# Kernel tuning notes

Hardware: AMD Instinct MI355X
Metric: run time of the kernel (lower is better)

## Reference

```python
import jax, jax.numpy as jnp
import numpy as np

N = 100000      # nodes
E = 1600000     # edges (avg degree 16)
IN = 128        # in_channels
H = 128         # hidden
C = 40          # num_classes
NCOMM = 1000    # number of communities


def setup_inputs() -> dict:
    key = jax.random.key(0)
    ks = jax.random.split(key, 6)
    x = jax.random.normal(ks[0], (N, IN), dtype=jnp.float32)
    edge_index = jax.random.randint(ks[1], (2, E), 0, N, dtype=jnp.int64)
    community = jax.random.randint(ks[2], (N,), 0, NCOMM, dtype=jnp.int64)
    W_in = jax.random.normal(ks[3], (2 * IN, H), dtype=jnp.float32) * 0.05
    b_in = jnp.zeros((H,), dtype=jnp.float32)
    W1 = jax.random.normal(ks[4], (H, H), dtype=jnp.float32) * 0.05
    b1 = jnp.zeros((H,), dtype=jnp.float32)
    W2 = jax.random.normal(ks[5], (H, C), dtype=jnp.float32) * 0.05
    b2 = jnp.zeros((C,), dtype=jnp.float32)
    return {"x": x, "edge_index": edge_index, "community": community,
            "W_in": W_in, "b_in": b_in, "W1": W1, "b1": b1, "W2": W2, "b2": b2}


def _gcn_conv(h, W, b, src, dst, n):
    """PyG GCNConv: transform, add self-loops, symmetric deg^-1/2 normalization."""
    hw = h @ W  # [n, out]
    deg = jax.ops.segment_sum(jnp.ones((src.shape[0],), hw.dtype), dst, num_segments=n) + 1.0  # +1 self-loop
    dis = jax.lax.rsqrt(deg)                      # deg >= 1 always
    norm = dis[src] * dis[dst]                    # [E]
    agg = jax.ops.segment_sum(hw[src] * norm[:, None], dst, num_segments=n)
    # self-loop contribution: norm_ii = dis[i]^2 = 1/deg[i]
    return agg + hw * (1.0 / deg)[:, None] + b


def reference(x, edge_index, community, W_in, b_in, W1, b1, W2, b2):
    n = x.shape[0]
    # CommunityPassing(aggr='mean'): per-community mean, broadcast back to nodes
    csum = jax.ops.segment_sum(x, community, num_segments=NCOMM)
    ccnt = jax.ops.segment_sum(jnp.ones((n,), x.dtype), community, num_segments=NCOMM)
    cmean = csum / jnp.maximum(ccnt, 1.0)[:, None]
    x_comm = cmean[community]                     # [n, IN]
    h = jnp.concatenate([x, x_comm], axis=-1)     # [n, 2*IN]
    h = jax.nn.relu(h @ W_in + b_in)              # dropout is identity at eval
    src, dst = edge_index[0], edge_index[1]
    h = jax.nn.relu(_gcn_conv(h, W1, b1, src, dst, n))
    out = _gcn_conv(h, W2, b2, src, dst, n)
    return out
```

## Files before the change

### kernel.cpp

```cpp
#include <hip/hip_runtime.h>
#include <cstdint>
#include <cstddef>

#define NNODES 100000
#define NEDGES 1600000
#define INCH   128
#define HID    128
#define NCLS   40
#define NCOMM_ 1000

typedef unsigned int uint32;
typedef unsigned short ushort16;
typedef short s16x8 __attribute__((ext_vector_type(8)));
typedef float f32x4 __attribute__((ext_vector_type(4)));

static __device__ __forceinline__ float4 ld4(const float* p){ return *reinterpret_cast<const float4*>(p); }

static __device__ __forceinline__ unsigned short f2b(float f){
  union{float f; uint32 u;} v; v.f=f;
  uint32 r = v.u + 0x7fffu + ((v.u>>16)&1u);
  return (unsigned short)(r>>16);
}
static __device__ __forceinline__ float b2f(unsigned short h){
  union{uint32 u; float f;} v; v.u = ((uint32)h)<<16; return v.f;
}
static __device__ __forceinline__ float lo16f(uint32 u){ return __int_as_float((int)(u<<16)); }
static __device__ __forceinline__ float hi16f(uint32 u){ return __int_as_float((int)(u&0xffff0000u)); }

static __device__ __forceinline__ void acc8(float* a, uint4 v, float nr){
  a[0]=fmaf(lo16f(v.x),nr,a[0]); a[1]=fmaf(hi16f(v.x),nr,a[1]);
  a[2]=fmaf(lo16f(v.y),nr,a[2]); a[3]=fmaf(hi16f(v.y),nr,a[3]);
  a[4]=fmaf(lo16f(v.z),nr,a[4]); a[5]=fmaf(hi16f(v.z),nr,a[5]);
  a[6]=fmaf(lo16f(v.w),nr,a[6]); a[7]=fmaf(hi16f(v.w),nr,a[7]);
}
static __device__ __forceinline__ void acc4(float* a, uint2 v, float nr){
  a[0]=fmaf(lo16f(v.x),nr,a[0]); a[1]=fmaf(hi16f(v.x),nr,a[1]);
  a[2]=fmaf(lo16f(v.y),nr,a[2]); a[3]=fmaf(hi16f(v.y),nr,a[3]);
}

__global__ void k_count(const int* __restrict__ ei, int* __restrict__ deg,
                        const int* __restrict__ comm, int* __restrict__ ccnt){
  int idx = blockIdx.x*blockDim.x + threadIdx.x;
  if (idx < NEDGES) atomicAdd(&deg[ei[NEDGES + idx]], 1);
  if (idx < NNODES) atomicAdd(&ccnt[comm[idx]], 1);
}

__global__ void k_scan1(const int* __restrict__ in, int n, int* __restrict__ part){
  int t=threadIdx.x, b=blockIdx.x;
  int base=b*1024+t*4, s=0;
  #pragma unroll
  for(int j=0;j<4;j++){ int i=base+j; if(i<n) s+=in[i]; }
  #pragma unroll
  for(int off=32;off>0;off>>=1) s+=__shfl_down(s,off,64);
  __shared__ int wm[4];
  if((t&63)==0) wm[t>>6]=s;
  __syncthreads();
  if(t==0) part[b]=wm[0]+wm[1]+wm[2]+wm[3];
}

__global__ void k_scan2(int* __restrict__ part, int P){
  __shared__ int sm[256];
  int t=threadIdx.x;
  int v=(t<P)?part[t]:0;
  sm[t]=v; __syncthreads();
  #pragma unroll
  for(int off=1;off<256;off<<=1){
    int u=(t>=off)?sm[t-off]:0;
    __syncthreads();
    sm[t]+=u;
    __syncthreads();
  }
  if(t<P) part[t]=(t==0)?0:sm[t-1];
  if(t==0) part[P]=sm[255];
}

__global__ void k_scan3(const int* __restrict__ in, int n, const int* __restrict__ part, int P,
                        int* __restrict__ out){
  int t=threadIdx.x,b=blockIdx.x;
  int base=b*1024+t*4;
  int v[4], ts=0;
  #pragma unroll
  for(int j=0;j<4;j++){ v[j]=(base+j<n)?in[base+j]:0; ts+=v[j]; }
  int lane=t&63, w=t>>6, sc=ts;
  #pragma unroll
  for(int off=1;off<64;off<<=1){ int u=__shfl_up(sc,off,64); if(lane>=off) sc+=u; }
  __shared__ int wm[4];
  if(lane==63) wm[w]=sc;
  __syncthreads();
  int woff=0;
  for(int i=0;i<w;i++) woff+=wm[i];
  int pos=part[b]+woff+sc-ts;
  #pragma unroll
  for(int j=0;j<4;j++){ if(base+j<n) out[base+j]=pos; pos+=v[j]; }
  if(b==0 && t==0) out[n]=part[P];
}

__global__ void k_nodeprep(const int* __restrict__ deg, float* __restrict__ dis, float* __restrict__ dinv){
  int i=blockIdx.x*blockDim.x+threadIdx.x;
  if(i<NNODES){ float d=(float)(deg[i]+1); dis[i]=rsqrtf(d); dinv[i]=1.0f/d; }
}

__global__ void k_fill_edges(const int* __restrict__ ei, const int* __restrict__ rp, int* __restrict__ fill,
                             const float* __restrict__ dis, int2* __restrict__ ep){
  int e=blockIdx.x*blockDim.x+threadIdx.x;
  if(e<NEDGES){
    int s=ei[e], d=ei[NEDGES+e];
    int p=rp[d]+atomicAdd(&fill[d],1);
    ep[p]=make_int2(s, __float_as_int(dis[s]));
  }
}

__global__ void k_fill_comm(const int* __restrict__ comm, const int* __restrict__ crow, int* __restrict__ cfill,
                            int* __restrict__ cnode){
  int i=blockIdx.x*blockDim.x+threadIdx.x;
  if(i<NNODES){
    int c=comm[i];
    int p=crow[c]+atomicAdd(&cfill[c],1);
    cnode[p]=i;
  }
}

__global__ void k_comm_mean(const float* __restrict__ x, const int* __restrict__ crow,
                            const int* __restrict__ cnode, float* __restrict__ cmean){
  int c=blockIdx.x; int f=threadIdx.x;
  int a=crow[c], b=crow[c+1];
  float s=0.f;
  for(int j=a;j<b;j++){
    int nd=cnode[j];
    s += x[(size_t)nd*INCH + f];
  }
  float cnt=(float)(b-a);
  cmean[(size_t)c*INCH + f] = s / fmaxf(cnt,1.0f);
}

__global__ void k_wprep(const float* __restrict__ W_in, const float* __restrict__ W1, const float* __restrict__ W2,
                        ushort16* __restrict__ Wt0h, ushort16* __restrict__ Wt0l,
                        ushort16* __restrict__ Wt1h, ushort16* __restrict__ Wt1l,
                        ushort16* __restrict__ Wt2h, ushort16* __restrict__ Wt2l){
  int t = blockIdx.x*256 + threadIdx.x;
  float v; ushort16* ph; ushort16* pl; int off;
  if(t < 32768){
    int n=t>>8, k=t&255; v=W_in[k*128+n]; ph=Wt0h; pl=Wt0l; off=t;
  } else if(t < 49152){
    int u=t-32768; int n=u>>7, k=u&127; v=W1[k*128+n]; ph=Wt1h; pl=Wt1l; off=u;
  } else if(t < 55296){
    int u=t-49152; int n=u>>7, k=u&127; v=(n<40)?W2[k*40+n]:0.f; ph=Wt2h; pl=Wt2l; off=u;
  } else return;
  unsigned short h=f2b(v); unsigned short lo=f2b(v-b2f(h));
  ph[off]=h; pl[off]=lo;
}

template<int K, bool CONCAT, bool BIAS, bool RELU>
__global__ __launch_bounds__(256) void k_mm128(const void* __restrict__ A0, const float* __restrict__ A1f,
                                               const int* __restrict__ comm,
                                               const ushort16* __restrict__ WtH, const ushort16* __restrict__ WtL,
                                               const float* __restrict__ bias,
                                               ushort16* __restrict__ out, int M){
  __shared__ __align__(16) ushort16 As[128*40];
  __shared__ __align__(16) ushort16 Bh[128*40];
  __shared__ __align__(16) ushort16 Bl[128*40];
  int t=threadIdx.x;
  int m0=blockIdx.x*128;
  int lane=t&63, w=t>>6;
  int g=lane>>4, r15=lane&15;

  f32x4 acc0[8], acc1[8];
  #pragma unroll
  for(int i=0;i<8;i++){ acc0[i]=(f32x4){0,0,0,0}; acc1[i]=(f32x4){0,0,0,0}; }

  int ar = t>>1, ko = (t&1)*16;

  for(int kc=0;kc<K;kc+=32){
    __syncthreads();
    {
      s16x8 q0, q1;
      int gr = m0 + ar;
      if(gr < M){
        if(CONCAT){
          const float* src = (kc<128) ? ((const float*)A0 + (size_t)gr*128 + kc + ko)
                                      : (A1f + (size_t)comm[gr]*128 + (kc-128) + ko);
          float4 p0=ld4(src), p1=ld4(src+4), p2=ld4(src+8), p3=ld4(src+12);
          q0[0]=(short)f2b(p0.x); q0[1]=(short)f2b(p0.y); q0[2]=(short)f2b(p0.z); q0[3]=(short)f2b(p0.w);
          q0[4]=(short)f2b(p1.x); q0[5]=(short)f2b(p1.y); q0[6]=(short)f2b(p1.z); q0[7]=(short)f2b(p1.w);
          q1[0]=(short)f2b(p2.x); q1[1]=(short)f2b(p2.y); q1[2]=(short)f2b(p2.z); q1[3]=(short)f2b(p2.w);
          q1[4]=(short)f2b(p3.x); q1[5]=(short)f2b(p3.y); q1[6]=(short)f2b(p3.z); q1[7]=(short)f2b(p3.w);
        } else {
          const ushort16* srcu = (const ushort16*)A0 + (size_t)gr*K + kc + ko;
          q0 = *(const s16x8*)srcu;
          q1 = *(const s16x8*)(srcu+8);
        }
      } else {
        q0=(s16x8){0,0,0,0,0,0,0,0}; q1=q0;
      }
      ushort16* dst=&As[ar*40+ko];
      *(s16x8*)dst=q0; *(s16x8*)(dst+8)=q1;
    }
    {
      const ushort16* sh=&WtH[(size_t)ar*K + kc + ko];
      s16x8 b0=*(const s16x8*)sh, b1=*(const s16x8*)(sh+8);
      ushort16* dh=&Bh[ar*40+ko];
      *(s16x8*)dh=b0; *(s16x8*)(dh+8)=b1;
      const ushort16* sl=&WtL[(size_t)ar*K + kc + ko];
      s16x8 c0=*(const s16x8*)sl, c1=*(const s16x8*)(sl+8);
      ushort16* dl=&Bl[ar*40+ko];
      *(s16x8*)dl=c0; *(s16x8*)(dl+8)=c1;
    }
    __syncthreads();
    s16x8 a0 = *(const s16x8*)&As[(w*32      + r15)*40 + g*8];
    s16x8 a1 = *(const s16x8*)&As[(w*32 + 16 + r15)*40 + g*8];
    #pragma unroll
    for(int tn=0;tn<8;tn++){
      s16x8 bh = *(const s16x8*)&Bh[(tn*16 + r15)*40 + g*8];
      s16x8 bl = *(const s16x8*)&Bl[(tn*16 + r15)*40 + g*8];
      acc0[tn] = __builtin_amdgcn_mfma_f32_16x16x32_bf16(a0, bh, acc0[tn], 0,0,0);
      acc0[tn] = __builtin_amdgcn_mfma_f32_16x16x32_bf16(a0, bl, acc0[tn], 0,0,0);
      acc1[tn] = __builtin_amdgcn_mfma_f32_16x16x32_bf16(a1, bh, acc1[tn], 0,0,0);
      acc1[tn] = __builtin_amdgcn_mfma_f32_16x16x32_bf16(a1, bl, acc1[tn], 0,0,0);
    }
  }

  #pragma unroll
  for(int tn=0;tn<8;tn++){
    int col = tn*16 + r15;
    float bv = BIAS ? bias[col] : 0.f;
    #pragma unroll
    for(int rr=0;rr<4;rr++){
      int row0 = m0 + w*32 + g*4 + rr;
      if(row0 < M){
        float v = acc0[tn][rr] + bv;
        if(RELU) v = fmaxf(v, 0.f);
        out[(size_t)row0*128 + col] = f2b(v);
      }
      int row1 = m0 + w*32 + 16 + g*4 + rr;
      if(row1 < M){
        float v = acc1[tn][rr] + bv;
        if(RELU) v = fmaxf(v, 0.f);
        out[(size_t)row1*128 + col] = f2b(v);
      }
    }
  }
}

__global__ __launch_bounds__(256) void k_mm40(const ushort16* __restrict__ A0,
                                              const ushort16* __restrict__ WtH, const ushort16* __restrict__ WtL,
                                              ushort16* __restrict__ out, int M){
  __shared__ __align__(16) ushort16 As[128*40];
  __shared__ __align__(16) ushort16 Bh[48*40];
  __shared__ __align__(16) ushort16 Bl[48*40];
  int t=threadIdx.x;
  int m0=blockIdx.x*128;
  int lane=t&63, w=t>>6;
  int g=lane>>4, r15=lane&15;

  f32x4 acc0[3], acc1[3];
  #pragma unroll
  for(int i=0;i<3;i++){ acc0[i]=(f32x4){0,0,0,0}; acc1[i]=(f32x4){0,0,0,0}; }

  int ar=t>>1, ko=(t&1)*16;

  for(int kc=0;kc<128;kc+=32){
    __syncthreads();
    {
      s16x8 q0,q1;
      int gr=m0+ar;
      if(gr<M){
        const ushort16* srcu = A0 + (size_t)gr*128 + kc + ko;
        q0=*(const s16x8*)srcu; q1=*(const s16x8*)(srcu+8);
      } else { q0=(s16x8){0,0,0,0,0,0,0,0}; q1=q0; }
      ushort16* dst=&As[ar*40+ko];
      *(s16x8*)dst=q0; *(s16x8*)(dst+8)=q1;
    }
    if(t<96){
      int n=t>>1, k2=(t&1)*16;
      const ushort16* sh=&WtH[(size_t)n*128 + kc + k2];
      s16x8 b0=*(const s16x8*)sh, b1=*(const s16x8*)(sh+8);
      ushort16* dh=&Bh[n*40+k2];
      *(s16x8*)dh=b0; *(s16x8*)(dh+8)=b1;
    } else if(t<192){
      int u=t-96; int n=u>>1, k2=(u&1)*16;
      const ushort16* sl=&WtL[(size_t)n*128 + kc + k2];
      s16x8 c0=*(const s16x8*)sl, c1=*(const s16x8*)(sl+8);
      ushort16* dl=&Bl[n*40+k2];
      *(s16x8*)dl=c0; *(s16x8*)(dl+8)=c1;
    }
    __syncthreads();
    s16x8 a0=*(const s16x8*)&As[(w*32      + r15)*40 + g*8];
    s16x8 a1=*(const s16x8*)&As[(w*32 + 16 + r15)*40 + g*8];
    #pragma unroll
    for(int tn=0;tn<3;tn++){
      s16x8 bh=*(const s16x8*)&Bh[(tn*16 + r15)*40 + g*8];
      s16x8 bl=*(const s16x8*)&Bl[(tn*16 + r15)*40 + g*8];
      acc0[tn]=__builtin_amdgcn_mfma_f32_16x16x32_bf16(a0,bh,acc0[tn],0,0,0);
      acc0[tn]=__builtin_amdgcn_mfma_f32_16x16x32_bf16(a0,bl,acc0[tn],0,0,0);
      acc1[tn]=__builtin_amdgcn_mfma_f32_16x16x32_bf16(a1,bh,acc1[tn],0,0,0);
      acc1[tn]=__builtin_amdgcn_mfma_f32_16x16x32_bf16(a1,bl,acc1[tn],0,0,0);
    }
  }
  #pragma unroll
  for(int tn=0;tn<3;tn++){
    int col=tn*16+r15;
    if(col<NCLS){
      #pragma unroll
      for(int rr=0;rr<4;rr++){
        int row0=m0+w*32+g*4+rr;
        if(row0<M) out[(size_t)row0*NCLS+col]=f2b(acc0[tn][rr]);
        int row1=m0+w*32+16+g*4+rr;
        if(row1<M) out[(size_t)row1*NCLS+col]=f2b(acc1[tn][rr]);
      }
    }
  }
}

__global__ __launch_bounds__(256) void k_agg_h(const uint4* __restrict__ hwv, const int* __restrict__ rp,
                                               const int2* __restrict__ ep,
                                               const float* __restrict__ dis, const float* __restrict__ dinv,
                                               const float* __restrict__ bias, uint4* __restrict__ h1v){
  int w=threadIdx.x>>6;
  int i=blockIdx.x*4+w;
  if(i>=NNODES) return;
  int lane=threadIdx.x&63;
  int g=lane>>4, f=lane&15;
  int e0=rp[i], e1=rp[i+1];
  float di=dis[i];
  float a[8]={0,0,0,0,0,0,0,0};
  int e=e0+g;
  for(; e+4<e1; e+=8){
    int2 r0=ep[e], r1=ep[e+4];
    float n0=di*__int_as_float(r0.y), n1=di*__int_as_float(r1.y);
    uint4 v0=hwv[(size_t)r0.x*16+f];
    uint4 v1=hwv[(size_t)r1.x*16+f];
    acc8(a,v0,n0); acc8(a,v1,n1);
  }
  if(e<e1){
    int2 r0=ep[e];
    float n0=di*__int_as_float(r0.y);
    uint4 v0=hwv[(size_t)r0.x*16+f];
    acc8(a,v0,n0);
  }
  #pragma unroll
  for(int k=0;k<8;k++){
    a[k]+=__shfl_xor(a[k],16);
    a[k]+=__shfl_xor(a[k],32);
  }
  if(g==0){
    uint4 sv=hwv[(size_t)i*16+f];
    float dv=dinv[i];
    float4 bA=*reinterpret_cast<const float4*>(&bias[8*f]);
    float4 bB=*reinterpret_cast<const float4*>(&bias[8*f+4]);
    float o0=fmaxf(fmaf(lo16f(sv.x),dv,a[0])+bA.x,0.f);
    float o1=fmaxf(fmaf(hi16f(sv.x),dv,a[1])+bA.y,0.f);
    float o2=fmaxf(fmaf(lo16f(sv.y),dv,a[2])+bA.z,0.f);
    float o3=fmaxf(fmaf(hi16f(sv.y),dv,a[3])+bA.w,0.f);
    float o4=fmaxf(fmaf(lo16f(sv.z),dv,a[4])+bB.x,0.f);
    float o5=fmaxf(fmaf(hi16f(sv.z),dv,a[5])+bB.y,0.f);
    float o6=fmaxf(fmaf(lo16f(sv.w),dv,a[6])+bB.z,0.f);
    float o7=fmaxf(fmaf(hi16f(sv.w),dv,a[7])+bB.w,0.f);
    uint4 o;
    o.x=((uint32)f2b(o1)<<16)|(uint32)f2b(o0);
    o.y=((uint32)f2b(o3)<<16)|(uint32)f2b(o2);
    o.z=((uint32)f2b(o5)<<16)|(uint32)f2b(o4);
    o.w=((uint32)f2b(o7)<<16)|(uint32)f2b(o6);
    h1v[(size_t)i*16+f]=o;
  }
}

__global__ __launch_bounds__(256) void k_agg_out(const uint2* __restrict__ hv, const int* __restrict__ rp,
                                                 const int2* __restrict__ ep,
                                                 const float* __restrict__ dis, const float* __restrict__ dinv,
                                                 const float* __restrict__ bias, float* __restrict__ out){
  int w=threadIdx.x>>6;
  int i=blockIdx.x*4+w;
  if(i>=NNODES) return;
  int lane=threadIdx.x&63;
  int g=lane>>4, f=lane&15;
  bool act=(f<10);
  int e0=rp[i], e1=rp[i+1];
  float di=dis[i];
  float a[4]={0,0,0,0};
  int e=e0+g;
  for(; e+4<e1; e+=8){
    int2 r0=ep[e], r1=ep[e+4];
    float n0=di*__int_as_float(r0.y), n1=di*__int_as_float(r1.y);
    if(act){
      uint2 v0=hv[(size_t)r0.x*10+f];
      uint2 v1=hv[(size_t)r1.x*10+f];
      acc4(a,v0,n0); acc4(a,v1,n1);
    }
  }
  if(e<e1){
    int2 r0=ep[e];
    float n0=di*__int_as_float(r0.y);
    if(act){
      uint2 v0=hv[(size_t)r0.x*10+f];
      acc4(a,v0,n0);
    }
  }
  #pragma unroll
  for(int k=0;k<4;k++){
    a[k]+=__shfl_xor(a[k],16);
    a[k]+=__shfl_xor(a[k],32);
  }
  if(g==0 && act){
    uint2 sv=hv[(size_t)i*10+f];
    float dv=dinv[i];
    float4 b=*reinterpret_cast<const float4*>(&bias[4*f]);
    float4 o;
    o.x=fmaf(lo16f(sv.x),dv,a[0])+b.x;
    o.y=fmaf(hi16f(sv.x),dv,a[1])+b.y;
    o.z=fmaf(lo16f(sv.y),dv,a[2])+b.z;
    o.w=fmaf(hi16f(sv.y),dv,a[3])+b.w;
    *reinterpret_cast<float4*>(&out[(size_t)i*40+4*f])=o;
  }
}

extern "C" void kernel_launch(void* const* d_in, const int* in_sizes, int n_in,
                              void* d_out, int out_size, void* d_ws, size_t ws_size,
                              hipStream_t stream) {
  const float* x    = (const float*)d_in[0];
  const int*   ei   = (const int*)  d_in[1];
  const int*   comm = (const int*)  d_in[2];
  const float* W_in = (const float*)d_in[3];
  const float* b_in = (const float*)d_in[4];
  const float* W1   = (const float*)d_in[5];
  const float* b1   = (const float*)d_in[6];
  const float* W2   = (const float*)d_in[7];
  const float* b2   = (const float*)d_in[8];
  float* out = (float*)d_out;

  char* base=(char*)d_ws; size_t off=0;
  auto alloc=[&](size_t bytes)->void*{ void* p=base+off; off=(off+bytes+255)&~(size_t)255; return p; };

  int* zz    =(int*)alloc((size_t)(2*NNODES+2*NCOMM_)*4);
  int* deg_i = zz;
  int* fill  = zz + NNODES;
  int* ccnt  = zz + 2*NNODES;
  int* cfill = zz + 2*NNODES + NCOMM_;
  int* rp    =(int*)alloc((size_t)(NNODES+1)*4);
  int* crow  =(int*)alloc((size_t)(NCOMM_+1)*4);
  int* partA =(int*)alloc(260*4);
  int* partB =(int*)alloc(16*4);
  int2* ep   =(int2*)alloc((size_t)NEDGES*8);
  int* cnode =(int*)alloc((size_t)NNODES*4);
  float* dis =(float*)alloc((size_t)NNODES*4);
  float* dinv=(float*)alloc((size_t)NNODES*4);
  float* cmean=(float*)alloc((size_t)NCOMM_*INCH*4);
  ushort16* h0 =(ushort16*)alloc((size_t)NNODES*HID*2);
  ushort16* hw =(ushort16*)alloc((size_t)NNODES*HID*2);
  ushort16* Wt0h=(ushort16*)alloc(32768*2);
  ushort16* Wt0l=(ushort16*)alloc(32768*2);
  ushort16* Wt1h=(ushort16*)alloc(16384*2);
  ushort16* Wt1l=(ushort16*)alloc(16384*2);
  ushort16* Wt2h=(ushort16*)alloc(6144*2);
  ushort16* Wt2l=(ushort16*)alloc(6144*2);

  hipMemsetAsync(zz, 0, (size_t)(2*NNODES+2*NCOMM_)*4, stream);

  int gE=(NEDGES+255)/256, gN=(NNODES+255)/256;
  k_count<<<gE,256,0,stream>>>(ei, deg_i, comm, ccnt);

  int PA=(NNODES+1023)/1024;
  k_scan1<<<PA,256,0,stream>>>(deg_i, NNODES, partA);
  k_scan2<<<1,256,0,stream>>>(partA, PA);
  k_scan3<<<PA,256,0,stream>>>(deg_i, NNODES, partA, PA, rp);

  int PB=(NCOMM_+1023)/1024;
  k_scan1<<<PB,256,0,stream>>>(ccnt, NCOMM_, partB);
  k_scan2<<<1,256,0,stream>>>(partB, PB);
  k_scan3<<<PB,256,0,stream>>>(ccnt, NCOMM_, partB, PB, crow);

  k_nodeprep<<<gN,256,0,stream>>>(deg_i, dis, dinv);
  k_fill_edges<<<gE,256,0,stream>>>(ei, rp, fill, dis, ep);
  k_fill_comm<<<gN,256,0,stream>>>(comm, crow, cfill, cnode);
  k_comm_mean<<<NCOMM_,128,0,stream>>>(x, crow, cnode, cmean);
  k_wprep<<<216,256,0,stream>>>(W_in, W1, W2, Wt0h, Wt0l, Wt1h, Wt1l, Wt2h, Wt2l);

  int gM=(NNODES+127)/128;
  k_mm128<256,true,true,true><<<gM,256,0,stream>>>(x, cmean, comm, Wt0h, Wt0l, b_in, h0, NNODES);
  k_mm128<128,false,false,false><<<gM,256,0,stream>>>(h0, nullptr, nullptr, Wt1h, Wt1l, nullptr, hw, NNODES);
  int gA=(NNODES+3)/4;
  k_agg_h<<<gA,256,0,stream>>>((const uint4*)hw, rp, ep, dis, dinv, b1, (uint4*)h0);
  k_mm40<<<gM,256,0,stream>>>(h0, Wt2h, Wt2l, hw, NNODES);
  k_agg_out<<<gA,256,0,stream>>>((const uint2*)hw, rp, ep, dis, dinv, b2, out);
}
```

Before: 535.0 us.

## Build CSR via two-level bucketed counting sort instead of global atomics

Replaces the global-atomic degree count, node-level scan and atomic edge scatter with a bucket counting sort. Edges are first histogrammed per block into 256-node buckets in shared memory, scanned, and scattered into bucket order. A per-bucket kernel then builds the local CSR, degrees and normalisation with shared-memory atomics. Edge records shrink from (src, dis) pairs to src only, with dis[src] gathered in the aggregation kernels, which trades smaller edge reads for an extra dependent load. The build adds a serial single-block scan and an intermediate edge buffer pass.

```diff
diff --git a/kernel.cpp b/kernel.cpp
--- a/kernel.cpp
+++ b/kernel.cpp
@@ -9,6 +9,11 @@
 #define NCLS   40
 #define NCOMM_ 1000
 
+#define NBLK  128
+#define EPB   (NEDGES/NBLK)
+#define NBUCK ((NNODES+255)/256)
+#define NCNT  (NBLK*NBUCK)
+
 typedef unsigned int uint32;
 typedef unsigned short ushort16;
 typedef short s16x8 __attribute__((ext_vector_type(8)));
@@ -38,11 +43,109 @@
   a[2]=fmaf(lo16f(v.y),nr,a[2]); a[3]=fmaf(hi16f(v.y),nr,a[3]);
 }
 
-__global__ void k_count(const int* __restrict__ ei, int* __restrict__ deg,
-                        const int* __restrict__ comm, int* __restrict__ ccnt){
-  int idx = blockIdx.x*blockDim.x + threadIdx.x;
-  if (idx < NEDGES) atomicAdd(&deg[ei[NEDGES + idx]], 1);
-  if (idx < NNODES) atomicAdd(&ccnt[comm[idx]], 1);
+__global__ void k_ccomm(const int* __restrict__ comm, int* __restrict__ ccnt){
+  int i=blockIdx.x*blockDim.x+threadIdx.x;
+  if(i<NNODES) atomicAdd(&ccnt[comm[i]],1);
+}
+
+__global__ __launch_bounds__(256) void k_bcnt(const int* __restrict__ ei, int* __restrict__ cnt){
+  __shared__ int h[NBUCK];
+  int t=threadIdx.x, blk=blockIdx.x;
+  for(int i=t;i<NBUCK;i+=256) h[i]=0;
+  __syncthreads();
+  int base=blk*EPB;
+  for(int j=t;j<EPB;j+=256){
+    int d=ei[NEDGES+base+j];
+    atomicAdd(&h[d>>8],1);
+  }
+  __syncthreads();
+  for(int i=t;i<NBUCK;i+=256) cnt[i*NBLK+blk]=h[i];
+}
+
+__global__ __launch_bounds__(1024) void k_bscan(int* __restrict__ cnt, int* __restrict__ brow,
+                                                int* __restrict__ rp){
+  __shared__ int sm[1024];
+  int t=threadIdx.x;
+  const int span=(NCNT+1023)/1024;
+  int base=t*span;
+  int s=0;
+  for(int j=0;j<span;j++){ int i=base+j; if(i<NCNT) s+=cnt[i]; }
+  sm[t]=s; __syncthreads();
+  #pragma unroll
+  for(int off=1;off<1024;off<<=1){
+    int u=(t>=off)?sm[t-off]:0;
+    __syncthreads();
+    sm[t]+=u;
+    __syncthreads();
+  }
+  int run=(t==0)?0:sm[t-1];
+  for(int j=0;j<span;j++){
+    int i=base+j;
+    if(i<NCNT){
+      int c=cnt[i];
+      cnt[i]=run;
+      if((i&(NBLK-1))==0) brow[i/NBLK]=run;
+      run+=c;
+    }
+  }
+  if(t==1023){ brow[NBUCK]=NEDGES; rp[NNODES]=NEDGES; }
+}
+
+__global__ __launch_bounds__(256) void k_bscatter(const int* __restrict__ ei, const int* __restrict__ cnt,
+                                                  int2* __restrict__ ebuf){
+  __shared__ int offs[NBUCK];
+  int t=threadIdx.x, blk=blockIdx.x;
+  for(int i=t;i<NBUCK;i+=256) offs[i]=cnt[i*NBLK+blk];
+  __syncthreads();
+  int base=blk*EPB;
+  for(int j=t;j<EPB;j+=256){
+    int e=base+j;
+    int s=ei[e], d=ei[NEDGES+e];
+    int p=atomicAdd(&offs[d>>8],1);
+    ebuf[p]=make_int2(s,d);
+  }
+}
+
+__global__ __launch_bounds__(256) void k_bcsr(const int2* __restrict__ ebuf, const int* __restrict__ brow,
+                                              int* __restrict__ rp, float* __restrict__ dis,
+                                              float* __restrict__ dinv, int* __restrict__ esrc){
+  __shared__ int lcnt[256], lrp[256], lfill[256];
+  int b=blockIdx.x, t=threadIdx.x;
+  int e0=brow[b], e1=brow[b+1];
+  int n0=b*256, nloc=min(256, NNODES-n0);
+  lcnt[t]=0;
+  __syncthreads();
+  for(int e=e0+t;e<e1;e+=256){
+    int d=ebuf[e].y;
+    atomicAdd(&lcnt[d&255],1);
+  }
+  __syncthreads();
+  lrp[t]=lcnt[t]; __syncthreads();
+  #pragma unroll
+  for(int off=1;off<256;off<<=1){
+    int u=(t>=off)?lrp[t-off]:0;
+    __syncthreads();
+    lrp[t]+=u;
+    __syncthreads();
+  }
+  int excl=lrp[t]-lcnt[t];
+  __syncthreads();
+  lrp[t]=e0+excl;
+  lfill[t]=0;
+  if(t<nloc){
+    int gid=n0+t;
+    rp[gid]=e0+excl;
+    float dd=(float)(lcnt[t]+1);
+    dis[gid]=rsqrtf(dd);
+    dinv[gid]=1.0f/dd;
+  }
+  __syncthreads();
+  for(int e=e0+t;e<e1;e+=256){
+    int2 r=ebuf[e];
+    int lr=r.y&255;
+    int slot=atomicAdd(&lfill[lr],1);
+    esrc[lrp[lr]+slot]=r.x;
+  }
 }
 
 __global__ void k_scan1(const int* __restrict__ in, int n, int* __restrict__ part){
@@ -93,21 +196,6 @@
   #pragma unroll
   for(int j=0;j<4;j++){ if(base+j<n) out[base+j]=pos; pos+=v[j]; }
   if(b==0 && t==0) out[n]=part[P];
-}
-
-__global__ void k_nodeprep(const int* __restrict__ deg, float* __restrict__ dis, float* __restrict__ dinv){
-  int i=blockIdx.x*blockDim.x+threadIdx.x;
-  if(i<NNODES){ float d=(float)(deg[i]+1); dis[i]=rsqrtf(d); dinv[i]=1.0f/d; }
-}
-
-__global__ void k_fill_edges(const int* __restrict__ ei, const int* __restrict__ rp, int* __restrict__ fill,
-                             const float* __restrict__ dis, int2* __restrict__ ep){
-  int e=blockIdx.x*blockDim.x+threadIdx.x;
-  if(e<NEDGES){
-    int s=ei[e], d=ei[NEDGES+e];
-    int p=rp[d]+atomicAdd(&fill[d],1);
-    ep[p]=make_int2(s, __float_as_int(dis[s]));
-  }
 }
 
 __global__ void k_fill_comm(const int* __restrict__ comm, const int* __restrict__ crow, int* __restrict__ cfill,
@@ -312,7 +400,7 @@
 }
 
 __global__ __launch_bounds__(256) void k_agg_h(const uint4* __restrict__ hwv, const int* __restrict__ rp,
-                                               const int2* __restrict__ ep,
+                                               const int* __restrict__ esrc,
                                                const float* __restrict__ dis, const float* __restrict__ dinv,
                                                const float* __restrict__ bias, uint4* __restrict__ h1v){
   int w=threadIdx.x>>6;
@@ -325,16 +413,16 @@
   float a[8]={0,0,0,0,0,0,0,0};
   int e=e0+g;
   for(; e+4<e1; e+=8){
-    int2 r0=ep[e], r1=ep[e+4];
-    float n0=di*__int_as_float(r0.y), n1=di*__int_as_float(r1.y);
-    uint4 v0=hwv[(size_t)r0.x*16+f];
-    uint4 v1=hwv[(size_t)r1.x*16+f];
+    int s0=esrc[e], s1=esrc[e+4];
+    float n0=di*dis[s0], n1=di*dis[s1];
+    uint4 v0=hwv[(size_t)s0*16+f];
+    uint4 v1=hwv[(size_t)s1*16+f];
     acc8(a,v0,n0); acc8(a,v1,n1);
   }
   if(e<e1){
-    int2 r0=ep[e];
-    float n0=di*__int_as_float(r0.y);
-    uint4 v0=hwv[(size_t)r0.x*16+f];
+    int s0=esrc[e];
+    float n0=di*dis[s0];
+    uint4 v0=hwv[(size_t)s0*16+f];
     acc8(a,v0,n0);
   }
   #pragma unroll
@@ -365,7 +453,7 @@
 }
 
 __global__ __launch_bounds__(256) void k_agg_out(const uint2* __restrict__ hv, const int* __restrict__ rp,
-                                                 const int2* __restrict__ ep,
+                                                 const int* __restrict__ esrc,
                                                  const float* __restrict__ dis, const float* __restrict__ dinv,
                                                  const float* __restrict__ bias, float* __restrict__ out){
   int w=threadIdx.x>>6;
@@ -379,19 +467,19 @@
   float a[4]={0,0,0,0};
   int e=e0+g;
   for(; e+4<e1; e+=8){
-    int2 r0=ep[e], r1=ep[e+4];
-    float n0=di*__int_as_float(r0.y), n1=di*__int_as_float(r1.y);
+    int s0=esrc[e], s1=esrc[e+4];
+    float n0=di*dis[s0], n1=di*dis[s1];
     if(act){
-      uint2 v0=hv[(size_t)r0.x*10+f];
-      uint2 v1=hv[(size_t)r1.x*10+f];
+      uint2 v0=hv[(size_t)s0*10+f];
+      uint2 v1=hv[(size_t)s1*10+f];
       acc4(a,v0,n0); acc4(a,v1,n1);
     }
   }
   if(e<e1){
-    int2 r0=ep[e];
-    float n0=di*__int_as_float(r0.y);
+    int s0=esrc[e];
+    float n0=di*dis[s0];
     if(act){
-      uint2 v0=hv[(size_t)r0.x*10+f];
+      uint2 v0=hv[(size_t)s0*10+f];
       acc4(a,v0,n0);
     }
   }
@@ -430,16 +518,16 @@
   char* base=(char*)d_ws; size_t off=0;
   auto alloc=[&](size_t bytes)->void*{ void* p=base+off; off=(off+bytes+255)&~(size_t)255; return p; };
 
-  int* zz    =(int*)alloc((size_t)(2*NNODES+2*NCOMM_)*4);
-  int* deg_i = zz;
-  int* fill  = zz + NNODES;
-  int* ccnt  = zz + 2*NNODES;
-  int* cfill = zz + 2*NNODES + NCOMM_;
+  int* zz    =(int*)alloc((size_t)(2*NCOMM_)*4);
+  int* ccnt  = zz;
+  int* cfill = zz + NCOMM_;
+  int* cnt   =(int*)alloc((size_t)NCNT*4);
+  int* brow  =(int*)alloc((size_t)(NBUCK+1)*4);
   int* rp    =(int*)alloc((size_t)(NNODES+1)*4);
   int* crow  =(int*)alloc((size_t)(NCOMM_+1)*4);
-  int* partA =(int*)alloc(260*4);
   int* partB =(int*)alloc(16*4);
-  int2* ep   =(int2*)alloc((size_t)NEDGES*8);
+  int2* ebuf =(int2*)alloc((size_t)NEDGES*8);
+  int* esrc  =(int*)alloc((size_t)NEDGES*4);
   int* cnode =(int*)alloc((size_t)NNODES*4);
   float* dis =(float*)alloc((size_t)NNODES*4);
   float* dinv=(float*)alloc((size_t)NNODES*4);
@@ -453,23 +541,20 @@
   ushort16* Wt2h=(ushort16*)alloc(6144*2);
   ushort16* Wt2l=(ushort16*)alloc(6144*2);
 
-  hipMemsetAsync(zz, 0, (size_t)(2*NNODES+2*NCOMM_)*4, stream);
-
-  int gE=(NEDGES+255)/256, gN=(NNODES+255)/256;
-  k_count<<<gE,256,0,stream>>>(ei, deg_i, comm, ccnt);
-
-  int PA=(NNODES+1023)/1024;
-  k_scan1<<<PA,256,0,stream>>>(deg_i, NNODES, partA);
-  k_scan2<<<1,256,0,stream>>>(partA, PA);
-  k_scan3<<<PA,256,0,stream>>>(deg_i, NNODES, partA, PA, rp);
-
+  hipMemsetAsync(zz, 0, (size_t)(2*NCOMM_)*4, stream);
+
+  int gN=(NNODES+255)/256;
+
+  k_bcnt    <<<NBLK,256,0,stream>>>(ei, cnt);
+  k_bscan   <<<1,1024,0,stream>>>(cnt, brow, rp);
+  k_bscatter<<<NBLK,256,0,stream>>>(ei, cnt, ebuf);
+  k_bcsr    <<<NBUCK,256,0,stream>>>(ebuf, brow, rp, dis, dinv, esrc);
+
+  k_ccomm<<<gN,256,0,stream>>>(comm, ccnt);
   int PB=(NCOMM_+1023)/1024;
   k_scan1<<<PB,256,0,stream>>>(ccnt, NCOMM_, partB);
   k_scan2<<<1,256,0,stream>>>(partB, PB);
   k_scan3<<<PB,256,0,stream>>>(ccnt, NCOMM_, partB, PB, crow);
-
-  k_nodeprep<<<gN,256,0,stream>>>(deg_i, dis, dinv);
-  k_fill_edges<<<gE,256,0,stream>>>(ei, rp, fill, dis, ep);
   k_fill_comm<<<gN,256,0,stream>>>(comm, crow, cfill, cnode);
   k_comm_mean<<<NCOMM_,128,0,stream>>>(x, crow, cnode, cmean);
   k_wprep<<<216,256,0,stream>>>(W_in, W1, W2, Wt0h, Wt0l, Wt1h, Wt1l, Wt2h, Wt2l);
@@ -478,7 +563,7 @@
   k_mm128<256,true,true,true><<<gM,256,0,stream>>>(x, cmean, comm, Wt0h, Wt0l, b_in, h0, NNODES);
   k_mm128<128,false,false,false><<<gM,256,0,stream>>>(h0, nullptr, nullptr, Wt1h, Wt1l, nullptr, hw, NNODES);
   int gA=(NNODES+3)/4;
-  k_agg_h<<<gA,256,0,stream>>>((const uint4*)hw, rp, ep, dis, dinv, b1, (uint4*)h0);
+  k_agg_h<<<gA,256,0,stream>>>((const uint4*)hw, rp, esrc, dis, dinv, b1, (uint4*)h0);
   k_mm40<<<gM,256,0,stream>>>(h0, Wt2h, Wt2l, hw, NNODES);
-  k_agg_out<<<gA,256,0,stream>>>((const uint2*)hw, rp, ep, dis, dinv, b2, out);
-}
+  k_agg_out<<<gA,256,0,stream>>>((const uint2*)hw, rp, esrc, dis, dinv, b2, out);
+}
```

Result: slower. 552.5 us (+3.3%).
